# Kernel tuning notes

Measured on AMD Instinct MI355X. Metric: run time of the kernel, lower is better.

## Reference

```python
import jax, jax.numpy as jnp
import numpy as np
from jax import lax

# Dims (match init_kwargs)
N, L = 64, 4500
K, G1 = 64, 7
CP, AP, G2 = 8, 8, 5
CSA, ASA, G3 = 8, 8, 3
N_ITERS = 3


def setup_inputs() -> dict:
    key = jax.random.key(0)
    k1, k2, k3, k4, k5 = jax.random.split(key, 5)
    x = jax.random.normal(k1, (N, 1, L), dtype=jnp.float32)
    conv1_w = jax.random.normal(k2, (K, 1, G1), dtype=jnp.float32) / np.sqrt(G1)
    psi_m_w = jax.random.normal(k3, (CP * AP, CP * AP, G2), dtype=jnp.float32) / np.sqrt(CP * AP * G2)
    psi_mA_w = jax.random.normal(k4, (CSA * ASA, 1, AP, G3), dtype=jnp.float32) / np.sqrt(AP * G3)
    psi_mA_b = jax.random.normal(k5, (CSA * ASA,), dtype=jnp.float32) * 0.01
    return {"x": x, "conv1_w": conv1_w, "psi_m_w": psi_m_w,
            "psi_mA_w": psi_mA_w, "psi_mA_b": psi_mA_b}


def _conv1d_same(x, w):
    # x: [N, Cin, L], w: [Cout, Cin, k]
    return lax.conv_general_dilated(x, w, window_strides=(1,), padding="SAME",
                                    dimension_numbers=("NCH", "OIH", "NCH"))


def _forward(x, conv1_w, psi_m_w, psi_mA_w, psi_mA_b):
    # conv1: [N,1,L] -> [N,K,L]
    h = _conv1d_same(x, conv1_w)
    # Cell_A psi_m: [N,K,L] -> [N,K,L]
    h = _conv1d_same(h, psi_m_w)
    # squash (as written in torch: sq_norm/(1+sq_norm) * X / sq_norm)
    sq = jnp.sum(h * h, axis=-1, keepdims=True)            # [N,K,1]
    h = (sq / (1.0 + sq)) * (h / sq)
    # Conv2d: [N,1,K,L] -> [N, CSA*ASA, K//AP, L], stride (AP,1), pad (0, G3//2)
    h = h[:, None, :, :]
    pad_a = (G3 - 1) // 2
    h = lax.conv_general_dilated(h, psi_mA_w, window_strides=(AP, 1),
                                 padding=[(0, 0), (pad_a, pad_a)],
                                 dimension_numbers=("NCHW", "OIHW", "NCHW"))
    h = h + psi_mA_b[None, :, None, None]                   # [N,64,8,L]
    # Dynamic routing over n_caps axis (dim -2)
    b = jnp.zeros(h.shape[:3] + (1,), dtype=h.dtype)        # [N,C,8,1]
    vj = None
    for _ in range(N_ITERS - 1):
        c = jax.nn.softmax(b, axis=-2)                      # softmax over n_caps
        sj = jnp.sum(c * h, axis=-2, keepdims=True)         # [N,C,1,L]
        sqn = jnp.sum(sj * sj, axis=-1, keepdims=True)      # [N,C,1,1]
        vj = sqn / (sqn + 1.0) * (sj / sqn)                 # [N,C,1,L]
        bj = jnp.einsum("ncil,ncjl->ncij", h, vj)           # [N,C,8,1]
        b = b + bj
    # vj.squeeze(-1) is a no-op (last dim is L); reshape to [N, CSA, ASA*L]
    return vj.reshape(-1, CSA, ASA * L)


def reference(x, conv1_w, psi_m_w, psi_mA_w, psi_mA_b):
    return _forward(x, conv1_w, psi_m_w, psi_mA_w, psi_mA_b)
```

## Files before the change

### kernel.cpp

```cpp
#include <hip/hip_runtime.h>
#include <math.h>

#define L_LEN 4500
#define KSPL 12
#define KT 128
#define TW 148
#define NTB 18
#define TLC 128
#define NTC 36
#define RS 72

typedef _Float16 half8 __attribute__((ext_vector_type(8)));
typedef float f32x16 __attribute__((ext_vector_type(16)));

__device__ __forceinline__ half8 mk_half8(unsigned int w0, unsigned int w1,
                                          unsigned int w2, unsigned int w3) {
    union { unsigned int u[4]; half8 h; } t;
    t.u[0] = w0; t.u[1] = w1; t.u[2] = w2; t.u[3] = w3;
    return t.h;
}
__device__ __forceinline__ half8 u4_half8(uint4 v) {
    union { uint4 u; half8 h; } t; t.u = v; return t.h;
}

#define LOPAIR(a, b) (((a) & 0xffffu) | ((b) << 16))
#define HIPAIR(a, b) (((a) >> 16) | ((b) & 0xffff0000u))

__global__ void prep_w2f_k(const float* __restrict__ w2,
                           unsigned int* __restrict__ w2fh,
                           unsigned int* __restrict__ w2fl,
                           float* __restrict__ rowsum) {
    int i = blockIdx.x * 256 + threadIdx.x;
    if (i < 4096) rowsum[i] = 0.f;
    if (i >= 10240) return;
    int w = i & 3;
    int t = i >> 2;
    int lane = t & 63; t >>= 6;
    int ks = t & 3; t >>= 2;
    int g = t % 5;
    int kh = t / 5;
    int k = kh * 32 + (lane & 31);
    int ci0 = ks * 16 + (lane >> 5) * 8 + w * 2;
    unsigned int hw = 0, lw = 0;
#pragma unroll
    for (int e = 0; e < 2; ++e) {
        float v = w2[(k * 64 + ci0 + e) * 5 + g];
        _Float16 hi = (_Float16)v;
        _Float16 lo = (_Float16)(v - (float)hi);
        unsigned short hb = __builtin_bit_cast(unsigned short, hi);
        unsigned short lb = __builtin_bit_cast(unsigned short, lo);
        hw |= ((unsigned int)hb) << (16 * e);
        lw |= ((unsigned int)lb) << (16 * e);
    }
    w2fh[i] = hw;
    w2fl[i] = lw;
}

__global__ __launch_bounds__(256, 2) void conv12_k(const float* __restrict__ x,
                                                   const float* __restrict__ w1,
                                                   const unsigned int* __restrict__ w2fh,
                                                   const unsigned int* __restrict__ w2fl,
                                                   float* __restrict__ h2,
                                                   float* __restrict__ rowsum) {
    __shared__ float xs[140];
    __shared__ __align__(16) _Float16 shh[132 * RS];
    __shared__ __align__(16) _Float16 shl[132 * RS];
    int b = blockIdx.x;
    int xcd = b & 7;
    int gi = xcd * 288 + (b >> 3);
    int n = gi / NTC;
    int t = gi - n * NTC;
    int l0 = t * TLC;
    int lane = threadIdx.x & 63;
    int wid = threadIdx.x >> 6;
    int kh = wid >> 1;
    int colhalf = wid & 1;
    uint4 WHr[20], WLr[20];
    {
        const uint4* WH = (const uint4*)w2fh;
        const uint4* WL = (const uint4*)w2fl;
#pragma unroll
        for (int g = 0; g < 5; ++g)
#pragma unroll
            for (int ks = 0; ks < 4; ++ks) {
                WHr[g * 4 + ks] = WH[((kh * 5 + g) * 4 + ks) * 64 + lane];
                WLr[g * 4 + ks] = WL[((kh * 5 + g) * 4 + ks) * 64 + lane];
            }
    }
    const float* xr = x + (size_t)n * L_LEN;
    if (threadIdx.x < 138) {
        int l = l0 - 5 + threadIdx.x;
        xs[threadIdx.x] = (l >= 0 && l < L_LEN) ? xr[l] : 0.f;
    }
    __syncthreads();
    {
        int ci = lane;
        float w[7];
#pragma unroll
        for (int g = 0; g < 7; ++g) w[g] = w1[ci * 7 + g];
        for (int tt = 0; tt < 33; ++tt) {
            int r = wid * 33 + tt;
            int l = l0 + r - 2;
            float a = 0.f;
            if (l >= 0 && l < L_LEN) {
#pragma unroll
                for (int g = 0; g < 7; ++g) a += w[g] * xs[r + g];
            }
            _Float16 hi = (_Float16)a;
            _Float16 lo = (_Float16)(a - (float)hi);
            shh[r * RS + ci] = hi;
            shl[r * RS + ci] = lo;
        }
    }
    __syncthreads();
    int col = lane & 31;
    int kg = lane >> 5;
    f32x16 acc[2];
#pragma unroll
    for (int ls = 0; ls < 2; ++ls)
#pragma unroll
        for (int i = 0; i < 16; ++i) acc[ls][i] = 0.f;
#pragma unroll
    for (int g = 0; g < 5; ++g) {
#pragma unroll
        for (int ks = 0; ks < 4; ++ks) {
            int off = ks * 16 + kg * 8;
            half8 Ah = u4_half8(WHr[g * 4 + ks]);
            half8 Al = u4_half8(WLr[g * 4 + ks]);
#pragma unroll
            for (int ls = 0; ls < 2; ++ls) {
                int rb = colhalf * 64 + ls * 32 + col + g;
                half8 bh = *(const half8*)&shh[rb * RS + off];
                half8 bl = *(const half8*)&shl[rb * RS + off];
                acc[ls] = __builtin_amdgcn_mfma_f32_32x32x16_f16(Al, bh, acc[ls], 0, 0, 0);
                acc[ls] = __builtin_amdgcn_mfma_f32_32x32x16_f16(Ah, bl, acc[ls], 0, 0, 0);
                acc[ls] = __builtin_amdgcn_mfma_f32_32x32x16_f16(Ah, bh, acc[ls], 0, 0, 0);
            }
        }
    }
#pragma unroll
    for (int ls = 0; ls < 2; ++ls) {
        int lcol = l0 + colhalf * 64 + ls * 32 + col;
        if (lcol < L_LEN) {
#pragma unroll
            for (int rg = 0; rg < 16; ++rg) {
                int k = kh * 32 + (rg & 3) + 8 * (rg >> 2) + 4 * kg;
                h2[((size_t)n * 64 + k) * L_LEN + lcol] = acc[ls][rg];
            }
        }
    }
#pragma unroll
    for (int rg = 0; rg < 16; ++rg) {
        float s1 = 0.f;
#pragma unroll
        for (int ls = 0; ls < 2; ++ls) {
            int lcol = l0 + colhalf * 64 + ls * 32 + col;
            if (lcol < L_LEN) s1 += acc[ls][rg];
        }
#pragma unroll
        for (int m = 16; m; m >>= 1) s1 += __shfl_xor(s1, m, 32);
        if (col == 0) {
            int k = kh * 32 + (rg & 3) + 8 * (rg >> 2) + 4 * kg;
            atomicAdd(&rowsum[n * 64 + k], s1);
        }
    }
}

__global__ __launch_bounds__(256, 3) void corr_k(const float* __restrict__ h2,
                                                 float* __restrict__ Rp) {
    __shared__ __align__(16) unsigned int hl[64 * TW];
    int bid = blockIdx.x;
    int xcd = bid & 7;
    int r8 = bid >> 3;
    int n = xcd * 8 + (r8 & 7);
    int s = r8 >> 3;
    const float* h2n = h2 + (size_t)n * 64 * L_LEN;

    int lane = threadIdx.x & 63;
    int wid = threadIdx.x >> 6;
    int a0 = (wid >> 1) * 32;
    int b0 = (wid & 1) * 32;
    int row31 = lane & 31;
    int g = lane >> 5;

    f32x16 acc[5];
#pragma unroll
    for (int d = 0; d < 5; ++d)
#pragma unroll
        for (int i = 0; i < 16; ++i) acc[d][i] = 0.f;

    int trow = threadIdx.x >> 2;
    int tc4 = threadIdx.x & 3;

    const unsigned int* arow = &hl[(a0 + row31) * TW + (g << 3)];
    const unsigned int* brow = &hl[(b0 + row31) * TW + (g << 3)];

    for (int tt = 0; tt < 3; ++tt) {
        int t = s + tt * KSPL;
        int l0 = t * KT;
        __syncthreads();
        for (int i = 0; i < 9; ++i) {
            int c = tc4 + (i << 2);
            int lbase = l0 - 8 + (c << 2);
            float v[4];
            if (lbase >= 0 && lbase + 3 < L_LEN) {
                float4 f = *(const float4*)(h2n + (size_t)trow * L_LEN + lbase);
                v[0] = f.x; v[1] = f.y; v[2] = f.z; v[3] = f.w;
            } else {
#pragma unroll
                for (int q = 0; q < 4; ++q) {
                    int l = lbase + q;
                    v[q] = (l >= 0 && l < L_LEN) ? h2n[(size_t)trow * L_LEN + l] : 0.f;
                }
            }
            unsigned int wv[4];
#pragma unroll
            for (int q = 0; q < 4; ++q) {
                float xv = v[q];
                _Float16 hi = (_Float16)xv;
                float hif = (float)hi;
                _Float16 lo = (_Float16)(xv - hif);
                unsigned short hb = __builtin_bit_cast(unsigned short, hi);
                unsigned short lb = __builtin_bit_cast(unsigned short, lo);
                wv[q] = (unsigned int)hb | ((unsigned int)lb << 16);
            }
            uint4 uu; uu.x = wv[0]; uu.y = wv[1]; uu.z = wv[2]; uu.w = wv[3];
            *(uint4*)&hl[trow * TW + (c << 2)] = uu;
        }
        __syncthreads();
#pragma unroll
        for (int ks = 0; ks < 8; ++ks) {
            const int u0 = 8 + ks * 16;
            uint4 va0 = *(const uint4*)(arow + u0);
            uint4 va1 = *(const uint4*)(arow + u0 + 4);
            uint4 vb0 = *(const uint4*)(brow + u0 - 4);
            uint4 vb1 = *(const uint4*)(brow + u0);
            uint4 vb2 = *(const uint4*)(brow + u0 + 4);
            uint4 vb3 = *(const uint4*)(brow + u0 + 8);
            unsigned int WA[8] = {va0.x, va0.y, va0.z, va0.w, va1.x, va1.y, va1.z, va1.w};
            unsigned int V[16] = {vb0.x, vb0.y, vb0.z, vb0.w, vb1.x, vb1.y, vb1.z, vb1.w,
                                  vb2.x, vb2.y, vb2.z, vb2.w, vb3.x, vb3.y, vb3.z, vb3.w};
            half8 Ahi = mk_half8(LOPAIR(WA[0], WA[1]), LOPAIR(WA[2], WA[3]),
                                 LOPAIR(WA[4], WA[5]), LOPAIR(WA[6], WA[7]));
            half8 Alo = mk_half8(HIPAIR(WA[0], WA[1]), HIPAIR(WA[2], WA[3]),
                                 HIPAIR(WA[4], WA[5]), HIPAIR(WA[6], WA[7]));
#pragma unroll
            for (int d = 0; d < 5; ++d) {
                half8 Bhi = mk_half8(LOPAIR(V[d + 2], V[d + 3]), LOPAIR(V[d + 4], V[d + 5]),
                                     LOPAIR(V[d + 6], V[d + 7]), LOPAIR(V[d + 8], V[d + 9]));
                half8 Blo = mk_half8(HIPAIR(V[d + 2], V[d + 3]), HIPAIR(V[d + 4], V[d + 5]),
                                     HIPAIR(V[d + 6], V[d + 7]), HIPAIR(V[d + 8], V[d + 9]));
                acc[d] = __builtin_amdgcn_mfma_f32_32x32x16_f16(Alo, Bhi, acc[d], 0, 0, 0);
                acc[d] = __builtin_amdgcn_mfma_f32_32x32x16_f16(Ahi, Blo, acc[d], 0, 0, 0);
                acc[d] = __builtin_amdgcn_mfma_f32_32x32x16_f16(Ahi, Bhi, acc[d], 0, 0, 0);
            }
        }
    }
    float* base = Rp + (size_t)(n * KSPL + s) * 20480;
#pragma unroll
    for (int d = 0; d < 5; ++d) {
#pragma unroll
        for (int rg = 0; rg < 16; ++rg) {
            int crow = (rg & 3) + 8 * (rg >> 2) + 4 * g;
            base[d * 4096 + (a0 + crow) * 64 + b0 + row31] = acc[d][rg];
        }
    }
}

__global__ __launch_bounds__(256) void redT_k(const float* __restrict__ Rp,
                                              float* __restrict__ Rsum2) {
    __shared__ float ldsA[1280];
    int n = blockIdx.x >> 4;
    int a0 = (blockIdx.x & 15) * 4;
    int tid = threadIdx.x;
    float sacc[5];
#pragma unroll
    for (int q = 0; q < 5; ++q) sacc[q] = 0.f;
    for (int s2 = 0; s2 < KSPL; ++s2) {
        const float* src = Rp + (size_t)(n * KSPL + s2) * 20480;
#pragma unroll
        for (int q = 0; q < 5; ++q) {
            int idx2 = q * 256 + tid;
            int aL = idx2 / 320;
            int r = idx2 - 320 * aL;
            int d = r >> 6;
            int bb = r & 63;
            sacc[q] += src[d * 4096 + (a0 + aL) * 64 + bb];
        }
    }
#pragma unroll
    for (int q = 0; q < 5; ++q) ldsA[q * 256 + tid] = sacc[q];
    __syncthreads();
    float* dst = Rsum2 + (size_t)n * 20480 + a0 * 320;
#pragma unroll
    for (int q = 0; q < 5; ++q) {
        int oidx = q * 256 + tid;
        int aL = oidx / 320;
        int rr = oidx - 320 * aL;
        int bb = rr / 5;
        int d = rr - 5 * bb;
        dst[oidx] = ldsA[aL * 320 + d * 64 + bb];
    }
}

__global__ __launch_bounds__(256) void mjk_k(const float* __restrict__ Rsum2,
                                             const float* __restrict__ h2,
                                             const float* __restrict__ wA,
                                             float* __restrict__ Mout) {
    __shared__ float Rsub[320];
    __shared__ float wsA[1536];
    __shared__ float s0a[8], s1a[8], inva[8], s0b[8], s1b[8], invb[8];
    __shared__ float Mp[256];
    int bid = blockIdx.x;
    int n = bid / 36;
    int ij = bid - n * 36;
    int i = 0, rem = ij;
    while (rem >= 8 - i) { rem -= 8 - i; ++i; }
    int j = i + rem;
    int tid = threadIdx.x;
    size_t rbase = (size_t)n * 20480;
    {
        size_t base = rbase + (size_t)(8 * i) * 320 + (size_t)(8 * j) * 5;
        for (int fidx = tid; fidx < 320; fidx += 256)
            Rsub[fidx] = Rsum2[base + (fidx / 40) * 320 + (fidx % 40)];
    }
    for (int q = tid; q < 1536; q += 256) wsA[q] = wA[q];
    if (tid < 8) {
        int a = 8 * i + tid;
        s0a[tid] = h2[((size_t)n * 64 + a) * L_LEN + 0];
        s1a[tid] = h2[((size_t)n * 64 + a) * L_LEN + (L_LEN - 1)];
        inva[tid] = 1.f / (1.f + Rsum2[rbase + a * 325 + 2]);
    } else if (tid < 16) {
        int b = 8 * j + (tid - 8);
        s0b[tid - 8] = h2[((size_t)n * 64 + b) * L_LEN + 0];
        s1b[tid - 8] = h2[((size_t)n * 64 + b) * L_LEN + (L_LEN - 1)];
        invb[tid - 8] = 1.f / (1.f + Rsum2[rbase + b * 325 + 2]);
    }
    __syncthreads();
    int c = tid & 63;
    int sub = tid >> 6;
    float acc = 0.f;
#pragma unroll
    for (int pl = 0; pl < 2; ++pl) {
        int p = sub * 2 + pl;
        float ia = inva[p];
        float w0 = wsA[c * 24 + p * 3], w1 = wsA[c * 24 + p * 3 + 1],
              w2v = wsA[c * 24 + p * 3 + 2];
        float e1a = s1a[p], e0a = s0a[p];
#pragma unroll
        for (int pp = 0; pp < 8; ++pp) {
            float q0 = wsA[c * 24 + pp * 3], q1 = wsA[c * 24 + pp * 3 + 1],
                  q2 = wsA[c * 24 + pp * 3 + 2];
            const float* R5 = &Rsub[(p * 8 + pp) * 5];
            float term = (w2v * q0) * R5[0]
                       + (w1 * q0 + w2v * q1) * R5[1]
                       + (w0 * q0 + w1 * q1 + w2v * q2) * R5[2]
                       + (w0 * q1 + w1 * q2) * R5[3]
                       + (w0 * q2) * R5[4]
                       - (w0 * q0) * (e1a * s1b[pp])
                       - (w2v * q2) * (e0a * s0b[pp]);
            acc += ia * invb[pp] * term;
        }
    }
    Mp[tid] = acc;
    __syncthreads();
    if (tid < 64)
        Mout[((size_t)n * 64 + tid) * 36 + ij] =
            Mp[tid] + Mp[tid + 64] + Mp[tid + 128] + Mp[tid + 192];
}

__global__ __launch_bounds__(64) void routing_k(const float* __restrict__ Mout,
                                                const float* __restrict__ Rsum2,
                                                const float* __restrict__ h2,
                                                const float* __restrict__ rowsum,
                                                const float* __restrict__ wA,
                                                const float* __restrict__ bA,
                                                float* __restrict__ coefb) {
    __shared__ float s0s[64], s1s[64], Ts[64], invs[64];
    int n = blockIdx.x;
    int c = threadIdx.x;
    {
        int a = c;
        s0s[a] = h2[((size_t)n * 64 + a) * L_LEN + 0];
        s1s[a] = h2[((size_t)n * 64 + a) * L_LEN + (L_LEN - 1)];
        Ts[a]  = rowsum[n * 64 + a];
        invs[a] = 1.f / (1.f + Rsum2[(size_t)n * 20480 + a * 325 + 2]);
    }
    __syncthreads();
    float wreg[24];
#pragma unroll
    for (int q = 0; q < 24; ++q) wreg[q] = wA[c * 24 + q];
    float bc = bA[c];
    float SG[8];
#pragma unroll
    for (int i = 0; i < 8; ++i) {
        float s = 0.f;
#pragma unroll
        for (int p = 0; p < 8; ++p) {
            int a = 8 * i + p;
            float Ta = Ts[a];
            s += invs[a] * (wreg[p * 3 + 0] * (Ta - s1s[a]) +
                            wreg[p * 3 + 1] * Ta +
                            wreg[p * 3 + 2] * (Ta - s0s[a]));
        }
        SG[i] = s;
    }
    const float* Mrow = Mout + ((size_t)n * 64 + c) * 36;
    float M[36];
    {
        int k2 = 0;
#pragma unroll
        for (int i = 0; i < 8; ++i)
#pragma unroll
            for (int j = i; j < 8; ++j, ++k2)
                M[k2] = Mrow[k2] + bc * (SG[i] + SG[j]) + 4500.f * bc * bc;
    }
    float rs[8];
#pragma unroll
    for (int i = 0; i < 8; ++i) rs[i] = 0.f;
    {
        int idx2 = 0;
#pragma unroll
        for (int i = 0; i < 8; ++i)
#pragma unroll
            for (int j = i; j < 8; ++j, ++idx2) {
                rs[i] += M[idx2];
                if (j > i) rs[j] += M[idx2];
            }
    }
    float sumAll = 0.f;
#pragma unroll
    for (int i = 0; i < 8; ++i) sumAll += rs[i];
    float sqn1 = sumAll * (1.f / 64.f);
    float binv = 1.f / (8.f * (1.f + sqn1));
    float bv[8], mx = -1e30f;
#pragma unroll
    for (int i = 0; i < 8; ++i) { bv[i] = rs[i] * binv; mx = fmaxf(mx, bv[i]); }
    float e[8], se = 0.f;
#pragma unroll
    for (int i = 0; i < 8; ++i) { e[i] = expf(bv[i] - mx); se += e[i]; }
    float sinv = 1.f / se;
    float ci_[8];
#pragma unroll
    for (int i = 0; i < 8; ++i) ci_[i] = e[i] * sinv;
    float sqn2 = 0.f;
    {
        int idx2 = 0;
#pragma unroll
        for (int i = 0; i < 8; ++i)
#pragma unroll
            for (int j = i; j < 8; ++j, ++idx2)
                sqn2 += ((j > i) ? 2.f : 1.f) * ci_[i] * ci_[j] * M[idx2];
    }
    float scale = 1.f / (1.f + sqn2);
#pragma unroll
    for (int i = 0; i < 8; ++i) coefb[((size_t)n * 64 + c) * 8 + i] = ci_[i] * scale;
}

__global__ __launch_bounds__(256) void weff_k(const float* __restrict__ coefb,
                                              const float* __restrict__ wA,
                                              const float* __restrict__ Rsum2,
                                              const float* __restrict__ bA,
                                              unsigned int* __restrict__ Wfh,
                                              unsigned int* __restrict__ Wfl,
                                              float* __restrict__ vbias) {
    __shared__ float invs[64];
    __shared__ float coefs[512];
    int n = blockIdx.x;
    if (threadIdx.x < 64)
        invs[threadIdx.x] =
            1.f / (1.f + Rsum2[(size_t)n * 20480 + threadIdx.x * 325 + 2]);
    for (int i = threadIdx.x; i < 512; i += 256) coefs[i] = coefb[(size_t)n * 512 + i];
    __syncthreads();
    for (int i = threadIdx.x; i < 6144; i += 256) {
        int w = i & 3;
        int t2 = i >> 2;
        int lane = t2 & 63; t2 >>= 6;
        int ks = t2 & 3; t2 >>= 2;
        int g = t2 % 3;
        int kh = t2 / 3;
        int k = kh * 32 + (lane & 31);
        int ci0 = ks * 16 + (lane >> 5) * 8 + w * 2;
        unsigned int hw = 0, lw = 0;
#pragma unroll
        for (int e = 0; e < 2; ++e) {
            int ci = ci0 + e;
            float v = coefs[k * 8 + (ci >> 3)] * wA[k * 24 + (ci & 7) * 3 + g] *
                      invs[ci] * 65536.f;
            _Float16 hi = (_Float16)v;
            _Float16 lo = (_Float16)(v - (float)hi);
            unsigned short hb = __builtin_bit_cast(unsigned short, hi);
            unsigned short lb = __builtin_bit_cast(unsigned short, lo);
            hw |= ((unsigned int)hb) << (16 * e);
            lw |= ((unsigned int)lb) << (16 * e);
        }
        Wfh[(size_t)n * 6144 + i] = hw;
        Wfl[(size_t)n * 6144 + i] = lw;
    }
    if (threadIdx.x < 64) {
        float s = 0.f;
#pragma unroll
        for (int i = 0; i < 8; ++i) s += coefb[((size_t)n * 64 + threadIdx.x) * 8 + i];
        vbias[n * 64 + threadIdx.x] = bA[threadIdx.x] * s;
    }
}

__global__ __launch_bounds__(256, 2) void outconv_k(const float* __restrict__ h2,
                                                    const unsigned int* __restrict__ Wfh,
                                                    const unsigned int* __restrict__ Wfl,
                                                    const float* __restrict__ vbias,
                                                    float* __restrict__ out) {
    __shared__ __align__(16) _Float16 shh[264 * RS];
    __shared__ __align__(16) _Float16 shl[264 * RS];
    __shared__ float vbs[64];
    int b = blockIdx.x;
    int xcd = b & 7;
    int gi = xcd * 144 + (b >> 3);
    int n = gi / NTB;
    int t = gi - n * NTB;
    int l0 = t * 256;
    const float* h2n = h2 + (size_t)n * 64 * L_LEN;
    if (threadIdx.x < 64) vbs[threadIdx.x] = vbias[n * 64 + threadIdx.x];
    {
        int trow = threadIdx.x >> 2;
        int tc4 = threadIdx.x & 3;
        const float* hrow = h2n + (size_t)trow * L_LEN;
        int lb = l0 - 4;
        for (int i = 0; i < 17; ++i) {
            int c = tc4 + 4 * i;
            if (c >= 66) break;
            int lbase = lb + 4 * c;
            float v[4];
            if (lbase >= 0 && lbase + 3 < L_LEN) {
                float4 f = *(const float4*)(hrow + lbase);
                v[0] = f.x; v[1] = f.y; v[2] = f.z; v[3] = f.w;
            } else {
#pragma unroll
                for (int q = 0; q < 4; ++q) {
                    int l = lbase + q;
                    v[q] = (l >= 0 && l < L_LEN) ? hrow[l] : 0.f;
                }
            }
            int r = 4 * c;
#pragma unroll
            for (int q = 0; q < 4; ++q) {
                _Float16 hi = (_Float16)v[q];
                _Float16 lo = (_Float16)(v[q] - (float)hi);
                shh[(r + q) * RS + trow] = hi;
                shl[(r + q) * RS + trow] = lo;
            }
        }
    }
    __syncthreads();
    int lane = threadIdx.x & 63;
    int wid = threadIdx.x >> 6;
    int col = lane & 31;
    int kg = lane >> 5;
    int lb0 = wid * 64 + col;
    f32x16 acc[2][2];
#pragma unroll
    for (int a1 = 0; a1 < 2; ++a1)
#pragma unroll
        for (int a2 = 0; a2 < 2; ++a2)
#pragma unroll
            for (int i = 0; i < 16; ++i) acc[a1][a2][i] = 0.f;
    const uint4* WH = (const uint4*)(Wfh + (size_t)n * 6144);
    const uint4* WL = (const uint4*)(Wfl + (size_t)n * 6144);
#pragma unroll
    for (int g = 0; g < 3; ++g) {
#pragma unroll
        for (int ks = 0; ks < 4; ++ks) {
            uint4 ah0 = WH[((0 * 3 + g) * 4 + ks) * 64 + lane];
            uint4 ah1 = WH[((1 * 3 + g) * 4 + ks) * 64 + lane];
            uint4 al0 = WL[((0 * 3 + g) * 4 + ks) * 64 + lane];
            uint4 al1 = WL[((1 * 3 + g) * 4 + ks) * 64 + lane];
            int off = ks * 16 + kg * 8;
            int rb = lb0 + g + 3;
            half8 bh0 = *(const half8*)&shh[rb * RS + off];
            half8 bl0 = *(const half8*)&shl[rb * RS + off];
            half8 bh1 = *(const half8*)&shh[(rb + 32) * RS + off];
            half8 bl1 = *(const half8*)&shl[(rb + 32) * RS + off];
            half8 Ah0 = u4_half8(ah0), Al0 = u4_half8(al0);
            half8 Ah1 = u4_half8(ah1), Al1 = u4_half8(al1);
            acc[0][0] = __builtin_amdgcn_mfma_f32_32x32x16_f16(Al0, bh0, acc[0][0], 0, 0, 0);
            acc[0][0] = __builtin_amdgcn_mfma_f32_32x32x16_f16(Ah0, bl0, acc[0][0], 0, 0, 0);
            acc[0][0] = __builtin_amdgcn_mfma_f32_32x32x16_f16(Ah0, bh0, acc[0][0], 0, 0, 0);
            acc[0][1] = __builtin_amdgcn_mfma_f32_32x32x16_f16(Al0, bh1, acc[0][1], 0, 0, 0);
            acc[0][1] = __builtin_amdgcn_mfma_f32_32x32x16_f16(Ah0, bl1, acc[0][1], 0, 0, 0);
            acc[0][1] = __builtin_amdgcn_mfma_f32_32x32x16_f16(Ah0, bh1, acc[0][1], 0, 0, 0);
            acc[1][0] = __builtin_amdgcn_mfma_f32_32x32x16_f16(Al1, bh0, acc[1][0], 0, 0, 0);
            acc[1][0] = __builtin_amdgcn_mfma_f32_32x32x16_f16(Ah1, bl0, acc[1][0], 0, 0, 0);
            acc[1][0] = __builtin_amdgcn_mfma_f32_32x32x16_f16(Ah1, bh0, acc[1][0], 0, 0, 0);
            acc[1][1] = __builtin_amdgcn_mfma_f32_32x32x16_f16(Al1, bh1, acc[1][1], 0, 0, 0);
            acc[1][1] = __builtin_amdgcn_mfma_f32_32x32x16_f16(Ah1, bl1, acc[1][1], 0, 0, 0);
            acc[1][1] = __builtin_amdgcn_mfma_f32_32x32x16_f16(Ah1, bh1, acc[1][1], 0, 0, 0);
        }
    }
    const float inv_scale = 1.f / 65536.f;
#pragma unroll
    for (int kh = 0; kh < 2; ++kh) {
#pragma unroll
        for (int ls = 0; ls < 2; ++ls) {
            int lcol = l0 + lb0 + ls * 32;
            if (lcol < L_LEN) {
#pragma unroll
                for (int rg = 0; rg < 16; ++rg) {
                    int k = kh * 32 + (rg & 3) + 8 * (rg >> 2) + 4 * kg;
                    out[((size_t)n * 64 + k) * L_LEN + lcol] =
                        acc[kh][ls][rg] * inv_scale + vbs[k];
                }
            }
        }
    }
}

extern "C" void kernel_launch(void* const* d_in, const int* in_sizes, int n_in,
                              void* d_out, int out_size, void* d_ws, size_t ws_size,
                              hipStream_t stream) {
    const float* x  = (const float*)d_in[0];
    const float* w1 = (const float*)d_in[1];
    const float* w2 = (const float*)d_in[2];
    const float* wA = (const float*)d_in[3];
    const float* bA = (const float*)d_in[4];
    float* out = (float*)d_out;
    char* ws = (char*)d_ws;
    const size_t HB = (size_t)64 * 64 * L_LEN * 4;
    float* h2     = (float*)(ws + HB);
    float* rowsum = (float*)(ws + 2 * HB + 16384);
    unsigned int* w2fh = (unsigned int*)(ws + 2 * HB + 32768);
    unsigned int* w2fl = (unsigned int*)(ws + 2 * HB + 32768 + 40960);
    float* Rp    = (float*)ws;
    float* Rsum2 = (float*)(ws + 62914560);
    float* coefb = (float*)(ws + 68157440);
    unsigned int* Wfh = (unsigned int*)(ws + 68288512);
    unsigned int* Wfl = (unsigned int*)(ws + 68288512 + 1572864);
    float* vbias = (float*)(ws + 71434240);
    float* Mout  = (float*)(ws + 71450624);

    prep_w2f_k<<<40, 256, 0, stream>>>(w2, w2fh, w2fl, rowsum);
    conv12_k<<<64 * NTC, 256, 0, stream>>>(x, w1, w2fh, w2fl, h2, rowsum);
    corr_k<<<64 * KSPL, 256, 0, stream>>>(h2, Rp);
    redT_k<<<64 * 16, 256, 0, stream>>>(Rp, Rsum2);
    mjk_k<<<64 * 36, 256, 0, stream>>>(Rsum2, h2, wA, Mout);
    routing_k<<<64, 64, 0, stream>>>(Mout, Rsum2, h2, rowsum, wA, bA, coefb);
    weff_k<<<64, 256, 0, stream>>>(coefb, wA, Rsum2, bA, Wfh, Wfl, vbias);
    outconv_k<<<64 * NTB, 256, 0, stream>>>(h2, Wfh, Wfl, vbias, out);
}
```

Before: 325.2 us.

## Make conv12 kernel persistent so weight fragments load once per block

Measured after the change: 347.7 us. 1.07x slower.

```diff
diff --git a/kernel.cpp b/kernel.cpp
--- a/kernel.cpp
+++ b/kernel.cpp
@@ -8,10 +8,12 @@
 #define NTB 18
 #define TLC 128
 #define NTC 36
+#define CBLK 512
 #define RS 72
 
 typedef _Float16 half8 __attribute__((ext_vector_type(8)));
 typedef float f32x16 __attribute__((ext_vector_type(16)));
+typedef int i32x4 __attribute__((ext_vector_type(4)));
 
 __device__ __forceinline__ half8 mk_half8(unsigned int w0, unsigned int w1,
                                           unsigned int w2, unsigned int w3) {
@@ -21,6 +23,9 @@
 }
 __device__ __forceinline__ half8 u4_half8(uint4 v) {
     union { uint4 u; half8 h; } t; t.u = v; return t.h;
+}
+__device__ __forceinline__ half8 i4_half8(i32x4 v) {
+    union { i32x4 u; half8 h; } t; t.u = v; return t.h;
 }
 
 #define LOPAIR(a, b) (((a) & 0xffffu) | ((b) << 16))
@@ -65,103 +70,106 @@
     __shared__ float xs[140];
     __shared__ __align__(16) _Float16 shh[132 * RS];
     __shared__ __align__(16) _Float16 shl[132 * RS];
-    int b = blockIdx.x;
-    int xcd = b & 7;
-    int gi = xcd * 288 + (b >> 3);
-    int n = gi / NTC;
-    int t = gi - n * NTC;
-    int l0 = t * TLC;
     int lane = threadIdx.x & 63;
     int wid = threadIdx.x >> 6;
     int kh = wid >> 1;
     int colhalf = wid & 1;
-    uint4 WHr[20], WLr[20];
-    {
-        const uint4* WH = (const uint4*)w2fh;
-        const uint4* WL = (const uint4*)w2fl;
-#pragma unroll
-        for (int g = 0; g < 5; ++g)
-#pragma unroll
-            for (int ks = 0; ks < 4; ++ks) {
-                WHr[g * 4 + ks] = WH[((kh * 5 + g) * 4 + ks) * 64 + lane];
-                WLr[g * 4 + ks] = WL[((kh * 5 + g) * 4 + ks) * 64 + lane];
-            }
-    }
-    const float* xr = x + (size_t)n * L_LEN;
-    if (threadIdx.x < 138) {
-        int l = l0 - 5 + threadIdx.x;
-        xs[threadIdx.x] = (l >= 0 && l < L_LEN) ? xr[l] : 0.f;
-    }
-    __syncthreads();
-    {
-        int ci = lane;
-        float w[7];
-#pragma unroll
-        for (int g = 0; g < 7; ++g) w[g] = w1[ci * 7 + g];
-        for (int tt = 0; tt < 33; ++tt) {
-            int r = wid * 33 + tt;
-            int l = l0 + r - 2;
-            float a = 0.f;
-            if (l >= 0 && l < L_LEN) {
-#pragma unroll
-                for (int g = 0; g < 7; ++g) a += w[g] * xs[r + g];
-            }
-            _Float16 hi = (_Float16)a;
-            _Float16 lo = (_Float16)(a - (float)hi);
-            shh[r * RS + ci] = hi;
-            shl[r * RS + ci] = lo;
-        }
-    }
-    __syncthreads();
     int col = lane & 31;
     int kg = lane >> 5;
-    f32x16 acc[2];
-#pragma unroll
-    for (int ls = 0; ls < 2; ++ls)
-#pragma unroll
-        for (int i = 0; i < 16; ++i) acc[ls][i] = 0.f;
-#pragma unroll
-    for (int g = 0; g < 5; ++g) {
-#pragma unroll
-        for (int ks = 0; ks < 4; ++ks) {
-            int off = ks * 16 + kg * 8;
-            half8 Ah = u4_half8(WHr[g * 4 + ks]);
-            half8 Al = u4_half8(WLr[g * 4 + ks]);
-#pragma unroll
-            for (int ls = 0; ls < 2; ++ls) {
-                int rb = colhalf * 64 + ls * 32 + col + g;
-                half8 bh = *(const half8*)&shh[rb * RS + off];
-                half8 bl = *(const half8*)&shl[rb * RS + off];
-                acc[ls] = __builtin_amdgcn_mfma_f32_32x32x16_f16(Al, bh, acc[ls], 0, 0, 0);
-                acc[ls] = __builtin_amdgcn_mfma_f32_32x32x16_f16(Ah, bl, acc[ls], 0, 0, 0);
-                acc[ls] = __builtin_amdgcn_mfma_f32_32x32x16_f16(Ah, bh, acc[ls], 0, 0, 0);
-            }
-        }
-    }
-#pragma unroll
-    for (int ls = 0; ls < 2; ++ls) {
-        int lcol = l0 + colhalf * 64 + ls * 32 + col;
-        if (lcol < L_LEN) {
-#pragma unroll
-            for (int rg = 0; rg < 16; ++rg) {
-                int k = kh * 32 + (rg & 3) + 8 * (rg >> 2) + 4 * kg;
-                h2[((size_t)n * 64 + k) * L_LEN + lcol] = acc[ls][rg];
-            }
-        }
-    }
-#pragma unroll
-    for (int rg = 0; rg < 16; ++rg) {
-        float s1 = 0.f;
+    i32x4 WHr[20], WLr[20];
+    {
+        const i32x4* WH = (const i32x4*)w2fh;
+        const i32x4* WL = (const i32x4*)w2fl;
+#pragma unroll
+        for (int q = 0; q < 20; ++q) {
+            WHr[q] = WH[(kh * 20 + q) * 64 + lane];
+            WLr[q] = WL[(kh * 20 + q) * 64 + lane];
+        }
+    }
+#pragma unroll
+    for (int q = 0; q < 20; ++q) {
+        asm volatile("" : "+v"(WHr[q]));
+        asm volatile("" : "+v"(WLr[q]));
+    }
+    float w1r[7];
+#pragma unroll
+    for (int g = 0; g < 7; ++g) w1r[g] = w1[lane * 7 + g];
+
+    for (int job = blockIdx.x; job < 64 * NTC; job += CBLK) {
+        int n = job / NTC;
+        int t = job - n * NTC;
+        int l0 = t * TLC;
+        __syncthreads();
+        const float* xr = x + (size_t)n * L_LEN;
+        if (threadIdx.x < 138) {
+            int l = l0 - 5 + threadIdx.x;
+            xs[threadIdx.x] = (l >= 0 && l < L_LEN) ? xr[l] : 0.f;
+        }
+        __syncthreads();
+        {
+            for (int tt = 0; tt < 33; ++tt) {
+                int r = wid * 33 + tt;
+                int l = l0 + r - 2;
+                float a = 0.f;
+                if (l >= 0 && l < L_LEN) {
+#pragma unroll
+                    for (int g = 0; g < 7; ++g) a += w1r[g] * xs[r + g];
+                }
+                _Float16 hi = (_Float16)a;
+                _Float16 lo = (_Float16)(a - (float)hi);
+                shh[r * RS + lane] = hi;
+                shl[r * RS + lane] = lo;
+            }
+        }
+        __syncthreads();
+        f32x16 acc[2];
+#pragma unroll
+        for (int ls = 0; ls < 2; ++ls)
+#pragma unroll
+            for (int i = 0; i < 16; ++i) acc[ls][i] = 0.f;
+#pragma unroll
+        for (int g = 0; g < 5; ++g) {
+#pragma unroll
+            for (int ks = 0; ks < 4; ++ks) {
+                int off = ks * 16 + kg * 8;
+                half8 Ah = i4_half8(WHr[g * 4 + ks]);
+                half8 Al = i4_half8(WLr[g * 4 + ks]);
+#pragma unroll
+                for (int ls = 0; ls < 2; ++ls) {
+                    int rb = colhalf * 64 + ls * 32 + col + g;
+                    half8 bh = *(const half8*)&shh[rb * RS + off];
+                    half8 bl = *(const half8*)&shl[rb * RS + off];
+                    acc[ls] = __builtin_amdgcn_mfma_f32_32x32x16_f16(Al, bh, acc[ls], 0, 0, 0);
+                    acc[ls] = __builtin_amdgcn_mfma_f32_32x32x16_f16(Ah, bl, acc[ls], 0, 0, 0);
+                    acc[ls] = __builtin_amdgcn_mfma_f32_32x32x16_f16(Ah, bh, acc[ls], 0, 0, 0);
+                }
+            }
+        }
 #pragma unroll
         for (int ls = 0; ls < 2; ++ls) {
             int lcol = l0 + colhalf * 64 + ls * 32 + col;
-            if (lcol < L_LEN) s1 += acc[ls][rg];
-        }
-#pragma unroll
-        for (int m = 16; m; m >>= 1) s1 += __shfl_xor(s1, m, 32);
-        if (col == 0) {
-            int k = kh * 32 + (rg & 3) + 8 * (rg >> 2) + 4 * kg;
-            atomicAdd(&rowsum[n * 64 + k], s1);
+            if (lcol < L_LEN) {
+#pragma unroll
+                for (int rg = 0; rg < 16; ++rg) {
+                    int k = kh * 32 + (rg & 3) + 8 * (rg >> 2) + 4 * kg;
+                    h2[((size_t)n * 64 + k) * L_LEN + lcol] = acc[ls][rg];
+                }
+            }
+        }
+#pragma unroll
+        for (int rg = 0; rg < 16; ++rg) {
+            float s1 = 0.f;
+#pragma unroll
+            for (int ls = 0; ls < 2; ++ls) {
+                int lcol = l0 + colhalf * 64 + ls * 32 + col;
+                if (lcol < L_LEN) s1 += acc[ls][rg];
+            }
+#pragma unroll
+            for (int m = 16; m; m >>= 1) s1 += __shfl_xor(s1, m, 32);
+            if (col == 0) {
+                int k = kh * 32 + (rg & 3) + 8 * (rg >> 2) + 4 * kg;
+                atomicAdd(&rowsum[n * 64 + k], s1);
+            }
         }
     }
 }
@@ -638,7 +646,7 @@
     float* Mout  = (float*)(ws + 71450624);
 
     prep_w2f_k<<<40, 256, 0, stream>>>(w2, w2fh, w2fl, rowsum);
-    conv12_k<<<64 * NTC, 256, 0, stream>>>(x, w1, w2fh, w2fl, h2, rowsum);
+    conv12_k<<<CBLK, 256, 0, stream>>>(x, w1, w2fh, w2fl, h2, rowsum);
     corr_k<<<64 * KSPL, 256, 0, stream>>>(h2, Rp);
     redT_k<<<64 * 16, 256, 0, stream>>>(Rp, Rsum2);
     mjk_k<<<64 * 36, 256, 0, stream>>>(Rsum2, h2, wA, Mout);
```
